# Kernel tuning notes

Hardware: AMD Instinct MI355X
Metric: run time of the kernel (lower is better)

Reference implementation:

```python
import jax, jax.numpy as jnp
import numpy as np

IN_C = 256
INTER_C = 128  # in_channels // reduction_ratio


def setup_inputs() -> dict:
    key = jax.random.key(0)
    ks = jax.random.split(key, 9)
    s = 1.0 / np.sqrt(IN_C)
    si = 1.0 / np.sqrt(INTER_C)
    return {
        "x": jax.random.normal(ks[0], (8, IN_C, 64, 64), dtype=jnp.float32),
        "g_w": jax.random.uniform(ks[1], (INTER_C, IN_C), jnp.float32, -s, s),
        "g_b": jax.random.uniform(ks[2], (INTER_C,), jnp.float32, -s, s),
        "theta_w": jax.random.uniform(ks[3], (INTER_C, IN_C), jnp.float32, -s, s),
        "theta_b": jax.random.uniform(ks[4], (INTER_C,), jnp.float32, -s, s),
        "phi_w": jax.random.uniform(ks[5], (INTER_C, IN_C), jnp.float32, -s, s),
        "phi_b": jax.random.uniform(ks[6], (INTER_C,), jnp.float32, -s, s),
        "W_w": jax.random.uniform(ks[7], (IN_C, INTER_C), jnp.float32, -si, si),
        "W_b": jax.random.uniform(ks[8], (IN_C,), jnp.float32, -si, si),
    }


def _conv1x1(x, w, b):
    # x: [b, cin, h, w]; w: [cout, cin] -> [b, cout, h, w]
    return jnp.einsum('oc,bchw->bohw', w, x) + b[None, :, None, None]


def reference(x, g_w, g_b, theta_w, theta_b, phi_w, phi_b, W_w, W_b):
    b, c, h, w = x.shape
    n = h * w
    g_x = _conv1x1(x, g_w, g_b).reshape(b, INTER_C, n)        # [b, i, n]
    theta_x = _conv1x1(x, theta_w, theta_b).reshape(b, INTER_C, n)
    phi_x = _conv1x1(x, phi_w, phi_b).reshape(b, INTER_C, n)
    # f[b, q, k] = sum_i theta[b, i, q] * phi[b, i, k]
    f = jnp.einsum('biq,bik->bqk', theta_x, phi_x)            # [b, n, n]
    f_div_C = jax.nn.softmax(f, axis=-1)
    # y[b, q, i] = sum_k f_div_C[b, q, k] * g_x[b, i, k]
    y = jnp.einsum('bqk,bik->biq', f_div_C, g_x)              # [b, i, n]
    y = y.reshape(b, INTER_C, h, w)
    W_y = _conv1x1(y, W_w, W_b)
    return W_y + x
```

## Files before the change

kernel.cpp:

```cpp
#include <hip/hip_runtime.h>
#include <hip/hip_bf16.h>
#include <stdint.h>

#define NB 8
#define CIN 256
#define IC 128
#define NP 4096

typedef __attribute__((ext_vector_type(8))) short s8v;
typedef __attribute__((ext_vector_type(4))) short s4v;
typedef __attribute__((ext_vector_type(16))) float f16v;
typedef __attribute__((ext_vector_type(4))) float f4v;

#define MFMA32(a, b, c) __builtin_amdgcn_mfma_f32_32x32x16_bf16(a, b, c, 0, 0, 0)

__device__ __forceinline__ unsigned short f2bf(float f) {
  union { float f; unsigned int u; } v; v.f = f;
  unsigned int u = v.u;
  return (unsigned short)((u + 0x7FFFu + ((u >> 16) & 1u)) >> 16);
}

__device__ __forceinline__ unsigned short f2bf_h(float f) {
  __hip_bfloat16 h = __float2bfloat16(f);
  union { __hip_bfloat16 h; unsigned short u; } cv; cv.h = h;
  return cv.u;
}

__device__ __forceinline__ float bf2f(short s) {
  union { unsigned int u; float f; } cv;
  cv.u = ((unsigned int)(unsigned short)s) << 16;
  return cv.f;
}

typedef const unsigned int __attribute__((address_space(1))) gas_u32;
typedef unsigned int __attribute__((address_space(3))) las_u32;
__device__ __forceinline__ void gload_lds16(const void* g, void* l) {
  __builtin_amdgcn_global_load_lds((gas_u32*)g, (las_u32*)l, 16, 0, 0);
}

__global__ __launch_bounds__(256) void k_conv3(const float* __restrict__ x,
    const float* __restrict__ thw, const float* __restrict__ thb,
    const float* __restrict__ phw, const float* __restrict__ phb,
    const float* __restrict__ gw,  const float* __restrict__ gb,
    unsigned short* __restrict__ Qg, unsigned short* __restrict__ Kg,
    unsigned short* __restrict__ Vtg) {
  __shared__ unsigned short X[64 * 256];
  __shared__ unsigned short T[64][72];
  const int t = threadIdx.x, lane = t & 63, wid = t >> 6;
  const int b = blockIdx.x & 7;
  const int p0 = (blockIdx.x >> 3) * 64;
  const int hl = lane >> 5;
  const float* xb = x + (size_t)b * CIN * NP + p0;
  const int cl = t >> 4;
  const int p4 = (t & 15) * 4;
  for (int sub = 0; sub < 4; ++sub) {
    const int c0 = sub * 64;
#pragma unroll
    for (int j = 0; j < 4; ++j) {
      const int cloc = cl + j * 16;
      const f4v v = *(const f4v*)(xb + (size_t)(c0 + cloc) * NP + p4);
      ushort4 u;
      u.x = f2bf(v[0]); u.y = f2bf(v[1]); u.z = f2bf(v[2]); u.w = f2bf(v[3]);
      *(ushort4*)&T[cloc][p4 ^ ((cloc & 7) * 8)] = u;
    }
    __syncthreads();
    const int p = t >> 2;
#pragma unroll
    for (int half = 0; half < 2; ++half) {
      const int cg = (t & 3) + half * 4;
      alignas(16) unsigned short outv[8];
#pragma unroll
      for (int k = 0; k < 8; ++k)
        outv[k] = T[cg * 8 + k][p ^ (k * 8)];
      const int cc = sub * 8 + cg;
      *(uint4*)&X[p * 256 + 8 * (cc ^ (2 * (p & 15)))] = *(const uint4*)outv;
    }
    __syncthreads();
  }
  const int orow = wid * 32 + (lane & 31);

  for (int mat = 0; mat < 3; ++mat) {
    const float* W  = (mat == 0) ? thw : ((mat == 1) ? phw : gw);
    const float* Bs = (mat == 0) ? thb : ((mat == 1) ? phb : gb);
    const float wsc = (mat == 0) ? 1.44269504f : 1.0f;
    s8v wf[16];
#pragma unroll
    for (int s = 0; s < 16; ++s) {
      const float* wp = W + (size_t)orow * CIN + hl * 8 + 16 * s;
      const f4v a = *(const f4v*)wp;
      const f4v c = *(const f4v*)(wp + 4);
      s8v f;
      f[0] = (short)f2bf(a[0] * wsc); f[1] = (short)f2bf(a[1] * wsc);
      f[2] = (short)f2bf(a[2] * wsc); f[3] = (short)f2bf(a[3] * wsc);
      f[4] = (short)f2bf(c[0] * wsc); f[5] = (short)f2bf(c[1] * wsc);
      f[6] = (short)f2bf(c[2] * wsc); f[7] = (short)f2bf(c[3] * wsc);
      wf[s] = f;
    }
    float br[16];
#pragma unroll
    for (int r = 0; r < 16; ++r)
      br[r] = Bs[wid * 32 + (r & 3) + 8 * (r >> 2) + 4 * hl] * wsc;

#pragma unroll
    for (int nt = 0; nt < 2; ++nt) {
      const int p = (lane & 31) + nt * 32;
      f16v acc;
#pragma unroll
      for (int i = 0; i < 16; ++i) acc[i] = 0.f;
#pragma unroll
      for (int s = 0; s < 16; ++s) {
        const int cc0 = hl + 2 * s;
        const s8v xf = *(const s8v*)&X[p * 256 + 8 * (cc0 ^ (2 * (p & 15)))];
        acc = MFMA32(wf[s], xf, acc);
      }
      if (mat < 2) {
        unsigned short* G = ((mat == 0) ? Qg : Kg) + ((size_t)b * NP + p0 + p) * IC;
#pragma unroll
        for (int grp = 0; grp < 4; ++grp) {
          const int d0 = wid * 32 + 8 * grp + 4 * hl;
          ushort4 u;
          u.x = f2bf(acc[grp * 4 + 0] + br[grp * 4 + 0]);
          u.y = f2bf(acc[grp * 4 + 1] + br[grp * 4 + 1]);
          u.z = f2bf(acc[grp * 4 + 2] + br[grp * 4 + 2]);
          u.w = f2bf(acc[grp * 4 + 3] + br[grp * 4 + 3]);
          *(ushort4*)(G + d0) = u;
        }
      } else {
        unsigned short* G = Vtg + (size_t)b * IC * NP + p0 + p;
#pragma unroll
        for (int r = 0; r < 16; ++r) {
          const int row = wid * 32 + (r & 3) + 8 * (r >> 2) + 4 * hl;
          G[(size_t)row * NP] = f2bf(acc[r] + br[r]);
        }
      }
    }
  }
}

__global__ __launch_bounds__(256, 2) void k_attn(const unsigned short* __restrict__ Qg,
    const unsigned short* __restrict__ Kg, const unsigned short* __restrict__ Vtg,
    unsigned short* __restrict__ Opart, float2* __restrict__ stats) {
  __shared__ unsigned short Klds[2][64 * 128];
  __shared__ unsigned short Vlds[2][128 * 68];
  const int t = threadIdx.x, lane = t & 63, wid = t >> 6;
  const int bid = blockIdx.x;
  const int b = bid & 7;
  const int q0 = ((bid >> 3) & 31) * 128;
  const int half = bid >> 8;
  const int it0 = half * 32;
  const int hl = lane >> 5;
  const int q = q0 + wid * 32 + (lane & 31);
  const unsigned short* Qp = Qg + (size_t)b * NP * IC + (size_t)q * IC;
  s8v qf[8];
#pragma unroll
  for (int s = 0; s < 8; ++s)
    qf[s] = *(const s8v*)(Qp + hl * 8 + 16 * s);
  f16v oa[4];
#pragma unroll
  for (int dt = 0; dt < 4; ++dt)
#pragma unroll
    for (int i = 0; i < 16; ++i) oa[dt][i] = 0.f;
  float m = -3.0e38f, lsum = 0.f;
  const unsigned short* Kb = Kg + (size_t)b * NP * IC;
  const unsigned short* Vb = Vtg + (size_t)b * IC * NP;
  const int ch = t & 7, dbase = t >> 3;

  uint4 vreg[4];
#pragma unroll
  for (int r = 0; r < 4; ++r) {
    const int ci = wid * 256 + r * 64 + lane;
    const int kv = ci >> 4, cc = ci & 15;
    gload_lds16(Kb + (size_t)(it0 * 64 + kv) * IC + 8 * (cc ^ (kv & 15)),
                (char*)&Klds[0][0] + wid * 4096 + r * 1024);
  }
  {
    const unsigned short* vs = Vb + it0 * 64 + ch * 8;
#pragma unroll
    for (int j = 0; j < 4; ++j)
      vreg[j] = *(const uint4*)(vs + (size_t)(dbase + j * 32) * NP);
#pragma unroll
    for (int j = 0; j < 4; ++j) {
      uint2* w0 = (uint2*)&Vlds[0][(dbase + j * 32) * 68 + ch * 8];
      w0[0] = make_uint2(vreg[j].x, vreg[j].y);
      w0[1] = make_uint2(vreg[j].z, vreg[j].w);
    }
  }
  __syncthreads();

  for (int it = it0; it < it0 + 32; ++it) {
    const int cur = it & 1;
    const bool more = (it < it0 + 31);
    if (more) {
      const int kv0n = (it + 1) * 64;
      const unsigned short* vs = Vb + kv0n + ch * 8;
#pragma unroll
      for (int j = 0; j < 4; ++j)
        vreg[j] = *(const uint4*)(vs + (size_t)(dbase + j * 32) * NP);
#pragma unroll
      for (int r = 0; r < 4; ++r) {
        const int ci = wid * 256 + r * 64 + lane;
        const int kv = ci >> 4, cc = ci & 15;
        gload_lds16(Kb + (size_t)(kv0n + kv) * IC + 8 * (cc ^ (kv & 15)),
                    (char*)&Klds[cur ^ 1][0] + wid * 4096 + r * 1024);
      }
    }
    f16v st0, st1;
#pragma unroll
    for (int i = 0; i < 16; ++i) { st0[i] = 0.f; st1[i] = 0.f; }
    __builtin_amdgcn_s_setprio(1);
#pragma unroll
    for (int s = 0; s < 8; ++s) {
      const int cc0 = hl + 2 * s;
      const int kva = lane & 31;
      const s8v ka  = *(const s8v*)&Klds[cur][kva * 128 + 8 * (cc0 ^ (kva & 15))];
      const s8v kb2 = *(const s8v*)&Klds[cur][(kva + 32) * 128 + 8 * (cc0 ^ (kva & 15))];
      st0 = MFMA32(ka, qf[s], st0);
      st1 = MFMA32(kb2, qf[s], st1);
    }
    __builtin_amdgcn_s_setprio(0);
    float tm[16];
#pragma unroll
    for (int i = 0; i < 16; ++i) tm[i] = fmaxf(st0[i], st1[i]);
#pragma unroll
    for (int w = 8; w >= 1; w >>= 1)
#pragma unroll
      for (int i = 0; i < 16; ++i) if (i < w) tm[i] = fmaxf(tm[i], tm[i + w]);
    float pmax = fmaxf(tm[0], __shfl_xor(tm[0], 32));
    if (__any(pmax > m + 8.f)) {
      const float mn = fmaxf(m, pmax);
      const float sc = __builtin_amdgcn_exp2f(m - mn);
      m = mn;
      lsum *= sc;
#pragma unroll
      for (int dt = 0; dt < 4; ++dt)
#pragma unroll
        for (int i = 0; i < 16; ++i) oa[dt][i] *= sc;
    }
#pragma unroll
    for (int i = 0; i < 16; ++i) st0[i] = __builtin_amdgcn_exp2f(st0[i] - m);
#pragma unroll
    for (int i = 0; i < 16; ++i) st1[i] = __builtin_amdgcn_exp2f(st1[i] - m);
    float ts[16];
#pragma unroll
    for (int i = 0; i < 16; ++i) ts[i] = st0[i] + st1[i];
#pragma unroll
    for (int w = 8; w >= 1; w >>= 1)
#pragma unroll
      for (int i = 0; i < 16; ++i) if (i < w) ts[i] += ts[i + w];
    lsum += ts[0] + __shfl_xor(ts[0], 32);
    s8v pf0, pf1, pf2, pf3;
#pragma unroll
    for (int i = 0; i < 8; ++i) {
      pf0[i] = (short)f2bf_h(st0[i]);
      pf1[i] = (short)f2bf_h(st0[8 + i]);
      pf2[i] = (short)f2bf_h(st1[i]);
      pf3[i] = (short)f2bf_h(st1[8 + i]);
    }
    if (more) {
#pragma unroll
      for (int j = 0; j < 4; ++j) {
        uint2* w0 = (uint2*)&Vlds[cur ^ 1][(dbase + j * 32) * 68 + ch * 8];
        w0[0] = make_uint2(vreg[j].x, vreg[j].y);
        w0[1] = make_uint2(vreg[j].z, vreg[j].w);
      }
    }
    __builtin_amdgcn_s_setprio(1);
#pragma unroll
    for (int ks = 0; ks < 4; ++ks) {
      const int k0 = 4 * hl + 16 * (ks & 1) + 32 * (ks >> 1);
      const s8v pcur = (ks == 0) ? pf0 : ((ks == 1) ? pf1 : ((ks == 2) ? pf2 : pf3));
#pragma unroll
      for (int dt = 0; dt < 4; ++dt) {
        const int d = dt * 32 + (lane & 31);
        const s4v va = *(const s4v*)&Vlds[cur][d * 68 + k0];
        const s4v vb2 = *(const s4v*)&Vlds[cur][d * 68 + k0 + 8];
        s8v vf;
        vf[0] = va[0]; vf[1] = va[1]; vf[2] = va[2]; vf[3] = va[3];
        vf[4] = vb2[0]; vf[5] = vb2[1]; vf[6] = vb2[2]; vf[7] = vb2[3];
        oa[dt] = MFMA32(vf, pcur, oa[dt]);
      }
    }
    __builtin_amdgcn_s_setprio(0);
    __syncthreads();
  }
  const float inv = 1.0f / lsum;
  unsigned short* Op = Opart + (size_t)half * NB * NP * IC + ((size_t)b * NP + q) * IC;
#pragma unroll
  for (int dt = 0; dt < 4; ++dt) {
#pragma unroll
    for (int grp = 0; grp < 4; ++grp) {
      const int d0 = dt * 32 + 8 * grp + 4 * hl;
      ushort4 u;
      u.x = f2bf_h(oa[dt][grp * 4 + 0] * inv);
      u.y = f2bf_h(oa[dt][grp * 4 + 1] * inv);
      u.z = f2bf_h(oa[dt][grp * 4 + 2] * inv);
      u.w = f2bf_h(oa[dt][grp * 4 + 3] * inv);
      *(ushort4*)(Op + d0) = u;
    }
  }
  if (hl == 0)
    stats[(size_t)half * NB * NP + (size_t)b * NP + q] = make_float2(m, lsum);
}

__global__ __launch_bounds__(256) void k_out(const unsigned short* __restrict__ Opart,
    const float2* __restrict__ stats,
    const float* __restrict__ Ww, const float* __restrict__ Wb,
    const float* __restrict__ x, float* __restrict__ out) {
  __shared__ unsigned short Y[64 * 128];
  const int t = threadIdx.x, lane = t & 63, wid = t >> 6;
  const int b = blockIdx.x & 7;
  const int p0 = (blockIdx.x >> 3) * 64;
  const int mt = blockIdx.y;
  const int hl = lane >> 5;
  {
    const int p = t >> 2;
    const int quarter = t & 3;
    const int ihb = quarter * 32;
    const int gq = p0 + p;
    const float2 s0 = stats[(size_t)b * NP + gq];
    const float2 s1 = stats[(size_t)NB * NP + (size_t)b * NP + gq];
    const float mm = fmaxf(s0.x, s1.x);
    const float w0 = s0.y * exp2f(s0.x - mm);
    const float w1 = s1.y * exp2f(s1.x - mm);
    const float rinv = 1.0f / (w0 + w1);
    const float a0 = w0 * rinv, a1 = w1 * rinv;
    const unsigned short* P0 = Opart + ((size_t)b * NP + gq) * IC + ihb;
    const unsigned short* P1 = Opart + (size_t)NB * NP * IC + ((size_t)b * NP + gq) * IC + ihb;
#pragma unroll
    for (int c8 = 0; c8 < 4; ++c8) {
      const s8v v0 = *(const s8v*)(P0 + c8 * 8);
      const s8v v1 = *(const s8v*)(P1 + c8 * 8);
      alignas(16) unsigned short o[8];
#pragma unroll
      for (int j = 0; j < 8; ++j)
        o[j] = f2bf_h(a0 * bf2f(v0[j]) + a1 * bf2f(v1[j]));
      const int cc = quarter * 4 + c8;
      *(uint4*)&Y[p * 128 + 8 * (cc ^ (p & 15))] = *(const uint4*)o;
    }
  }
  const int orow = mt * 128 + wid * 32 + (lane & 31);
  s8v wf[8];
#pragma unroll
  for (int s = 0; s < 8; ++s) {
    const float* wp = Ww + (size_t)orow * IC + hl * 8 + 16 * s;
    const f4v a = *(const f4v*)wp;
    const f4v c = *(const f4v*)(wp + 4);
    s8v f;
    f[0] = (short)f2bf(a[0]); f[1] = (short)f2bf(a[1]);
    f[2] = (short)f2bf(a[2]); f[3] = (short)f2bf(a[3]);
    f[4] = (short)f2bf(c[0]); f[5] = (short)f2bf(c[1]);
    f[6] = (short)f2bf(c[2]); f[7] = (short)f2bf(c[3]);
    wf[s] = f;
  }
  float br[16];
#pragma unroll
  for (int r = 0; r < 16; ++r)
    br[r] = Wb[mt * 128 + wid * 32 + (r & 3) + 8 * (r >> 2) + 4 * hl];
  __syncthreads();
#pragma unroll
  for (int nt = 0; nt < 2; ++nt) {
    const int p = (lane & 31) + nt * 32;
    f16v acc;
#pragma unroll
    for (int i = 0; i < 16; ++i) acc[i] = 0.f;
#pragma unroll
    for (int s = 0; s < 8; ++s) {
      const int cc0 = hl + 2 * s;
      const s8v yf = *(const s8v*)&Y[p * 128 + 8 * (cc0 ^ (p & 15))];
      acc = MFMA32(wf[s], yf, acc);
    }
    const size_t pidx = (size_t)b * CIN * NP + (size_t)(p0 + p);
#pragma unroll
    for (int r = 0; r < 16; ++r) {
      const int row = mt * 128 + wid * 32 + (r & 3) + 8 * (r >> 2) + 4 * hl;
      const size_t idx = pidx + (size_t)row * NP;
      out[idx] = acc[r] + br[r] + x[idx];
    }
  }
}

extern "C" void kernel_launch(void* const* d_in, const int* in_sizes, int n_in,
                              void* d_out, int out_size, void* d_ws, size_t ws_size,
                              hipStream_t stream) {
  const float* x   = (const float*)d_in[0];
  const float* gw  = (const float*)d_in[1];
  const float* gb  = (const float*)d_in[2];
  const float* thw = (const float*)d_in[3];
  const float* thb = (const float*)d_in[4];
  const float* phw = (const float*)d_in[5];
  const float* phb = (const float*)d_in[6];
  const float* Ww  = (const float*)d_in[7];
  const float* Wb  = (const float*)d_in[8];
  float* out = (float*)d_out;

  unsigned short* ws  = (unsigned short*)d_ws;
  unsigned short* Opart = ws;
  unsigned short* Qg  = ws + 8388608;
  unsigned short* Kg  = Qg + 4194304;
  unsigned short* Vtg = Kg + 4194304;
  float2* stats = (float2*)(Vtg + 4194304);

  k_conv3<<<dim3(512), dim3(256), 0, stream>>>(x, thw, thb, phw, phb, gw, gb,
                                               Qg, Kg, Vtg);
  k_attn<<<dim3(512), dim3(256), 0, stream>>>(Qg, Kg, Vtg, Opart, stats);
  k_out<<<dim3(512, 2), dim3(256), 0, stream>>>(Opart, stats, Ww, Wb, x, out);
}
```

Measured before the change: 151.0 us.

## Swizzle V tile in LDS for single 16-byte reads, split QK accumulators, merge k_out halves

The V tile in LDS now has a row stride of 72 with an XOR swizzle, so each MFMA B-operand comes from one 16-byte LDS read instead of two 8-byte reads plus register shuffling. The QK^T MFMA chain is split into two independent accumulator pairs that are summed afterwards, which shortens the MFMA dependency chain. k_out now handles both 128-row output halves in one block, looping over them, instead of using a second grid dimension. That avoids recombining the two attention partials and rebuilding the Y tile twice, but each block does more serial work and the grid is half the size.

```diff
diff --git a/kernel.cpp b/kernel.cpp
--- a/kernel.cpp
+++ b/kernel.cpp
@@ -8,7 +8,6 @@
 #define NP 4096
 
 typedef __attribute__((ext_vector_type(8))) short s8v;
-typedef __attribute__((ext_vector_type(4))) short s4v;
 typedef __attribute__((ext_vector_type(16))) float f16v;
 typedef __attribute__((ext_vector_type(4))) float f4v;
 
@@ -141,7 +140,7 @@
     const unsigned short* __restrict__ Kg, const unsigned short* __restrict__ Vtg,
     unsigned short* __restrict__ Opart, float2* __restrict__ stats) {
   __shared__ unsigned short Klds[2][64 * 128];
-  __shared__ unsigned short Vlds[2][128 * 68];
+  __shared__ unsigned short Vlds[2][128 * 72];
   const int t = threadIdx.x, lane = t & 63, wid = t >> 6;
   const int bid = blockIdx.x;
   const int b = bid & 7;
@@ -164,6 +163,10 @@
   const unsigned short* Kb = Kg + (size_t)b * NP * IC;
   const unsigned short* Vb = Vtg + (size_t)b * IC * NP;
   const int ch = t & 7, dbase = t >> 3;
+  const int jb2 = 16 * (ch >> 1) + 4 * (ch & 1);
+  const int vswz = ((dbase >> 3) & 1) * 8;
+  const int o1 = jb2 ^ vswz;
+  const int o2 = (jb2 + 8) ^ vswz;
 
   uint4 vreg[4];
 #pragma unroll
@@ -180,9 +183,9 @@
       vreg[j] = *(const uint4*)(vs + (size_t)(dbase + j * 32) * NP);
 #pragma unroll
     for (int j = 0; j < 4; ++j) {
-      uint2* w0 = (uint2*)&Vlds[0][(dbase + j * 32) * 68 + ch * 8];
-      w0[0] = make_uint2(vreg[j].x, vreg[j].y);
-      w0[1] = make_uint2(vreg[j].z, vreg[j].w);
+      const int d = dbase + j * 32;
+      *(uint2*)&Vlds[0][d * 72 + o1] = make_uint2(vreg[j].x, vreg[j].y);
+      *(uint2*)&Vlds[0][d * 72 + o2] = make_uint2(vreg[j].z, vreg[j].w);
     }
   }
   __syncthreads();
@@ -204,20 +207,26 @@
                     (char*)&Klds[cur ^ 1][0] + wid * 4096 + r * 1024);
       }
     }
-    f16v st0, st1;
-#pragma unroll
-    for (int i = 0; i < 16; ++i) { st0[i] = 0.f; st1[i] = 0.f; }
+    f16v st0a, st0b, st1a, st1b;
+#pragma unroll
+    for (int i = 0; i < 16; ++i) { st0a[i] = 0.f; st0b[i] = 0.f; st1a[i] = 0.f; st1b[i] = 0.f; }
+    const int kva = lane & 31;
     __builtin_amdgcn_s_setprio(1);
 #pragma unroll
-    for (int s = 0; s < 8; ++s) {
+    for (int s = 0; s < 8; s += 2) {
       const int cc0 = hl + 2 * s;
-      const int kva = lane & 31;
-      const s8v ka  = *(const s8v*)&Klds[cur][kva * 128 + 8 * (cc0 ^ (kva & 15))];
-      const s8v kb2 = *(const s8v*)&Klds[cur][(kva + 32) * 128 + 8 * (cc0 ^ (kva & 15))];
-      st0 = MFMA32(ka, qf[s], st0);
-      st1 = MFMA32(kb2, qf[s], st1);
+      const s8v ka0 = *(const s8v*)&Klds[cur][kva * 128 + 8 * (cc0 ^ (kva & 15))];
+      const s8v kb0 = *(const s8v*)&Klds[cur][(kva + 32) * 128 + 8 * (cc0 ^ (kva & 15))];
+      const s8v ka1 = *(const s8v*)&Klds[cur][kva * 128 + 8 * ((cc0 + 2) ^ (kva & 15))];
+      const s8v kb1 = *(const s8v*)&Klds[cur][(kva + 32) * 128 + 8 * ((cc0 + 2) ^ (kva & 15))];
+      st0a = MFMA32(ka0, qf[s], st0a);
+      st1a = MFMA32(kb0, qf[s], st1a);
+      st0b = MFMA32(ka1, qf[s + 1], st0b);
+      st1b = MFMA32(kb1, qf[s + 1], st1b);
     }
     __builtin_amdgcn_s_setprio(0);
+    f16v st0 = st0a + st0b;
+    f16v st1 = st1a + st1b;
     float tm[16];
 #pragma unroll
     for (int i = 0; i < 16; ++i) tm[i] = fmaxf(st0[i], st1[i]);
@@ -259,24 +268,21 @@
     if (more) {
 #pragma unroll
       for (int j = 0; j < 4; ++j) {
-        uint2* w0 = (uint2*)&Vlds[cur ^ 1][(dbase + j * 32) * 68 + ch * 8];
-        w0[0] = make_uint2(vreg[j].x, vreg[j].y);
-        w0[1] = make_uint2(vreg[j].z, vreg[j].w);
+        const int d = dbase + j * 32;
+        *(uint2*)&Vlds[cur ^ 1][d * 72 + o1] = make_uint2(vreg[j].x, vreg[j].y);
+        *(uint2*)&Vlds[cur ^ 1][d * 72 + o2] = make_uint2(vreg[j].z, vreg[j].w);
       }
     }
     __builtin_amdgcn_s_setprio(1);
 #pragma unroll
     for (int ks = 0; ks < 4; ++ks) {
-      const int k0 = 4 * hl + 16 * (ks & 1) + 32 * (ks >> 1);
       const s8v pcur = (ks == 0) ? pf0 : ((ks == 1) ? pf1 : ((ks == 2) ? pf2 : pf3));
+      const int voff = 16 * ks + 8 * hl;
 #pragma unroll
       for (int dt = 0; dt < 4; ++dt) {
         const int d = dt * 32 + (lane & 31);
-        const s4v va = *(const s4v*)&Vlds[cur][d * 68 + k0];
-        const s4v vb2 = *(const s4v*)&Vlds[cur][d * 68 + k0 + 8];
-        s8v vf;
-        vf[0] = va[0]; vf[1] = va[1]; vf[2] = va[2]; vf[3] = va[3];
-        vf[4] = vb2[0]; vf[5] = vb2[1]; vf[6] = vb2[2]; vf[7] = vb2[3];
+        const int rsw = ((d >> 3) & 1) * 8;
+        const s8v vf = *(const s8v*)&Vlds[cur][d * 72 + (voff ^ rsw)];
         oa[dt] = MFMA32(vf, pcur, oa[dt]);
       }
     }
@@ -310,7 +316,6 @@
   const int t = threadIdx.x, lane = t & 63, wid = t >> 6;
   const int b = blockIdx.x & 7;
   const int p0 = (blockIdx.x >> 3) * 64;
-  const int mt = blockIdx.y;
   const int hl = lane >> 5;
   {
     const int p = t >> 2;
@@ -338,43 +343,45 @@
       *(uint4*)&Y[p * 128 + 8 * (cc ^ (p & 15))] = *(const uint4*)o;
     }
   }
-  const int orow = mt * 128 + wid * 32 + (lane & 31);
-  s8v wf[8];
-#pragma unroll
-  for (int s = 0; s < 8; ++s) {
-    const float* wp = Ww + (size_t)orow * IC + hl * 8 + 16 * s;
-    const f4v a = *(const f4v*)wp;
-    const f4v c = *(const f4v*)(wp + 4);
-    s8v f;
-    f[0] = (short)f2bf(a[0]); f[1] = (short)f2bf(a[1]);
-    f[2] = (short)f2bf(a[2]); f[3] = (short)f2bf(a[3]);
-    f[4] = (short)f2bf(c[0]); f[5] = (short)f2bf(c[1]);
-    f[6] = (short)f2bf(c[2]); f[7] = (short)f2bf(c[3]);
-    wf[s] = f;
-  }
-  float br[16];
-#pragma unroll
-  for (int r = 0; r < 16; ++r)
-    br[r] = Wb[mt * 128 + wid * 32 + (r & 3) + 8 * (r >> 2) + 4 * hl];
   __syncthreads();
-#pragma unroll
-  for (int nt = 0; nt < 2; ++nt) {
-    const int p = (lane & 31) + nt * 32;
-    f16v acc;
-#pragma unroll
-    for (int i = 0; i < 16; ++i) acc[i] = 0.f;
+  for (int mt = 0; mt < 2; ++mt) {
+    const int orow = mt * 128 + wid * 32 + (lane & 31);
+    s8v wf[8];
 #pragma unroll
     for (int s = 0; s < 8; ++s) {
-      const int cc0 = hl + 2 * s;
-      const s8v yf = *(const s8v*)&Y[p * 128 + 8 * (cc0 ^ (p & 15))];
-      acc = MFMA32(wf[s], yf, acc);
-    }
-    const size_t pidx = (size_t)b * CIN * NP + (size_t)(p0 + p);
-#pragma unroll
-    for (int r = 0; r < 16; ++r) {
-      const int row = mt * 128 + wid * 32 + (r & 3) + 8 * (r >> 2) + 4 * hl;
-      const size_t idx = pidx + (size_t)row * NP;
-      out[idx] = acc[r] + br[r] + x[idx];
+      const float* wp = Ww + (size_t)orow * IC + hl * 8 + 16 * s;
+      const f4v a = *(const f4v*)wp;
+      const f4v c = *(const f4v*)(wp + 4);
+      s8v f;
+      f[0] = (short)f2bf(a[0]); f[1] = (short)f2bf(a[1]);
+      f[2] = (short)f2bf(a[2]); f[3] = (short)f2bf(a[3]);
+      f[4] = (short)f2bf(c[0]); f[5] = (short)f2bf(c[1]);
+      f[6] = (short)f2bf(c[2]); f[7] = (short)f2bf(c[3]);
+      wf[s] = f;
+    }
+    float br[16];
+#pragma unroll
+    for (int r = 0; r < 16; ++r)
+      br[r] = Wb[mt * 128 + wid * 32 + (r & 3) + 8 * (r >> 2) + 4 * hl];
+#pragma unroll
+    for (int nt = 0; nt < 2; ++nt) {
+      const int p = (lane & 31) + nt * 32;
+      f16v acc;
+#pragma unroll
+      for (int i = 0; i < 16; ++i) acc[i] = 0.f;
+#pragma unroll
+      for (int s = 0; s < 8; ++s) {
+        const int cc0 = hl + 2 * s;
+        const s8v yf = *(const s8v*)&Y[p * 128 + 8 * (cc0 ^ (p & 15))];
+        acc = MFMA32(wf[s], yf, acc);
+      }
+      const size_t pidx = (size_t)b * CIN * NP + (size_t)(p0 + p);
+#pragma unroll
+      for (int r = 0; r < 16; ++r) {
+        const int row = mt * 128 + wid * 32 + (r & 3) + 8 * (r >> 2) + 4 * hl;
+        const size_t idx = pidx + (size_t)row * NP;
+        out[idx] = acc[r] + br[r] + x[idx];
+      }
     }
   }
 }
@@ -403,5 +410,5 @@
   k_conv3<<<dim3(512), dim3(256), 0, stream>>>(x, thw, thb, phw, phb, gw, gb,
                                                Qg, Kg, Vtg);
   k_attn<<<dim3(512), dim3(256), 0, stream>>>(Qg, Kg, Vtg, Opart, stats);
-  k_out<<<dim3(512, 2), dim3(256), 0, stream>>>(Opart, stats, Ww, Wb, x, out);
-}
+  k_out<<<dim3(512), dim3(256), 0, stream>>>(Opart, stats, Ww, Wb, x, out);
+}
```

After: 148.6 us. No clear change (-1.6%).
